# Kernel tuning notes

Measured on AMD Instinct MI355X. Metric: run time of the kernel, lower is better.

Reference implementation:

```python
import jax, jax.numpy as jnp
import numpy as np
from jax.scipy.special import logsumexp

TEMPERATURE = 0.1
EPS = 1e-8  # matches torch F.cosine_similarity eps


def setup_inputs() -> dict:
    key = jax.random.key(0)
    k1, k2 = jax.random.split(key)
    N, D, NUM_CLASSES = 8192, 256, 64
    embeddings = jax.random.normal(k1, (N, D), dtype=jnp.float32)
    target = jax.random.randint(k2, (N,), 0, NUM_CLASSES, dtype=jnp.int64)
    return {"embeddings": embeddings, "target": target}


def reference(embeddings, target):
    N = target.shape[0]
    # cosine similarity: normalize rows, then a single GEMM for all pairs
    norms = jnp.linalg.norm(embeddings, axis=-1, keepdims=True)
    e = embeddings / jnp.maximum(norms, EPS)
    sim = (e @ e.T) / TEMPERATURE  # [N, N]

    pos = target[:, None] == target[None, :]  # [N, N] bool, incl. diagonal
    diag = jnp.eye(N, dtype=bool)
    neg_inf = jnp.asarray(-jnp.inf, dtype=sim.dtype)

    # denominator: negatives only (positives masked to -inf)
    lse_neg = logsumexp(jnp.where(pos, neg_inf, sim), axis=1)
    # numerator: positives excluding self (diagonal masked to -inf)
    lse_pos = logsumexp(jnp.where(pos & ~diag, sim, neg_inf), axis=1)

    loss = lse_neg - lse_pos
    return loss.sum()
```

## Files before the change

### kernel.cpp

```cpp
#include <hip/hip_runtime.h>
#include <hip/hip_bf16.h>
#include <stdint.h>
#include <math.h>

#define NROWS 8192
#define DIM   256
#define RB    256
#define BI    128
#define JSUB  64
#define NBJS  8
#define JBLK  (JSUB*NBJS)
#define NG    (NROWS/JBLK)
#define NIT   (NROWS/BI)
#define CAP   256

typedef __attribute__((ext_vector_type(4)))  int   int4v;
typedef __attribute__((ext_vector_type(8)))  int   int8v;
typedef __attribute__((ext_vector_type(16))) float floatx16;

typedef const __attribute__((address_space(1))) uint32_t gas_u32;
typedef __attribute__((address_space(3))) uint32_t las_u32;

#define SCALE_1_16 0x7B7B7B7B
#define L2E10      14.4269504088896f

#if __has_builtin(__builtin_amdgcn_exp2f)
#define EXP2(x) __builtin_amdgcn_exp2f(x)
#else
#define EXP2(x) exp2f(x)
#endif

__device__ __forceinline__ void gload_lds16(const void* g, void* l) {
    __builtin_amdgcn_global_load_lds((gas_u32*)(uintptr_t)g,
                                     (las_u32*)(uintptr_t)l, 16, 0, 0);
}

__global__ __launch_bounds__(256) void normalize_kernel(const float* __restrict__ emb,
                                                        uint32_t* __restrict__ e8,
                                                        float* __restrict__ out)
{
    if (blockIdx.x == 0 && threadIdx.x == 0) *out = 0.f;
    int row  = blockIdx.x * 4 + (threadIdx.x >> 6);
    int lane = threadIdx.x & 63;
    const float4* rowp = (const float4*)(emb + (size_t)row * DIM);
    float4 v = rowp[lane];
    float ss = v.x*v.x + v.y*v.y + v.z*v.z + v.w*v.w;
    #pragma unroll
    for (int off = 32; off > 0; off >>= 1)
        ss += __shfl_xor(ss, off, 64);
    float inv = 16.0f / fmaxf(sqrtf(ss), 1e-8f);
    int r = __builtin_amdgcn_cvt_pk_fp8_f32(v.x * inv, v.y * inv, 0, false);
    r     = __builtin_amdgcn_cvt_pk_fp8_f32(v.z * inv, v.w * inv, r, true);
    e8[(size_t)row * (DIM / 4) + lane] = (uint32_t)r;
}

__global__ __launch_bounds__(256) void pos_kernel(const uint8_t* __restrict__ e8,
                                                  const int* __restrict__ tgt,
                                                  float* __restrict__ sp)
{
    __shared__ uint8_t rows[CAP * RB];
    __shared__ int idx[CAP];
    __shared__ int cnt;

    const int c    = blockIdx.x;
    const int tid  = threadIdx.x;
    const int wave = tid >> 6;
    const int lane = tid & 63;
    const int col  = lane & 31;
    const int h    = lane >> 5;

    if (tid == 0) cnt = 0;
    __syncthreads();
    for (int base = 0; base < NROWS; base += 256) {
        int j = base + tid;
        if (tgt[j] == c) {
            int p = atomicAdd(&cnt, 1);
            if (p < CAP) idx[p] = j;
        }
    }
    __syncthreads();
    const int M  = min(cnt, CAP);
    const int Mp = (M + 31) & ~31;

    const int nslots = M * 16;
    for (int g = wave; g * 64 < nslots; g += 4) {
        int s  = g * 64 + lane;
        int r  = s >> 4;
        int rc = min(r, M - 1);
        int lc = (s & 15) ^ (r & 15);
        gload_lds16(e8 + (size_t)idx[rc] * RB + lc * 16, rows + g * 1024);
    }
    __syncthreads();
    for (int s = M * 16 + tid; s < Mp * 16; s += 256)
        *(int4v*)(rows + (size_t)s * 16) = (int4v){0, 0, 0, 0};
    __syncthreads();

    const int xm = col & 15;
    int poff[4];
    #pragma unroll
    for (int s = 0; s < 4; ++s)
        poff[s] = ((s * 4 + h * 2) ^ xm) << 4;

    for (int bt = wave; bt * 32 < Mp; bt += 4) {
        const int b = bt * 32 + col;
        const uint8_t* pb = rows + (size_t)b * RB;
        int8v bfr[4];
        #pragma unroll
        for (int s = 0; s < 4; ++s) {
            int4v lo = *(const int4v*)(pb + poff[s]);
            int4v hi = *(const int4v*)(pb + (poff[s] ^ 16));
            bfr[s] = __builtin_shufflevector(lo, hi, 0, 1, 2, 3, 4, 5, 6, 7);
        }
        float psum = 0.f;
        for (int at = 0; at * 32 < Mp; ++at) {
            const uint8_t* pa = rows + (size_t)(at * 32 + col) * RB;
            floatx16 acc = (floatx16){0.f,0.f,0.f,0.f,0.f,0.f,0.f,0.f,
                                      0.f,0.f,0.f,0.f,0.f,0.f,0.f,0.f};
            #pragma unroll
            for (int s = 0; s < 4; ++s) {
                int4v lo = *(const int4v*)(pa + poff[s]);
                int4v hi = *(const int4v*)(pa + (poff[s] ^ 16));
                int8v af = __builtin_shufflevector(lo, hi, 0, 1, 2, 3, 4, 5, 6, 7);
                acc = __builtin_amdgcn_mfma_scale_f32_32x32x64_f8f6f4(
                    af, bfr[s], acc, 0, 0, 0, SCALE_1_16, 0, SCALE_1_16);
            }
            #pragma unroll
            for (int rq = 0; rq < 4; ++rq)
                #pragma unroll
                for (int r2 = 0; r2 < 4; ++r2) {
                    const int a = at * 32 + rq * 8 + h * 4 + r2;
                    float v = EXP2(fmaf(L2E10, acc[rq * 4 + r2], -L2E10));
                    psum += (a != b && a < M) ? v : 0.f;
                }
        }
        psum += __shfl_xor(psum, 32, 64);
        if (h == 0 && b < M) sp[idx[b]] = psum;
    }
}

template<bool DIAG>
__device__ __forceinline__ void epi(const floatx16 acc[2],
                                    int jbs, int h, int ic0, float& ts)
{
    #pragma unroll
    for (int jt = 0; jt < 2; ++jt)
        #pragma unroll
        for (int rq = 0; rq < 4; ++rq)
            #pragma unroll
            for (int r2 = 0; r2 < 4; ++r2) {
                float v = EXP2(fmaf(L2E10, acc[jt][rq * 4 + r2], -L2E10));
                if (DIAG) {
                    const int jg_ = jbs + jt * 32 + rq * 8 + h * 4 + r2;
                    if (jg_ == ic0) v = 0.f;
                }
                ts += v;
            }
}

__global__ __launch_bounds__(256, 4) void tile_kernel(const uint8_t* __restrict__ e8,
                                                      float* __restrict__ pts)
{
    __shared__ uint8_t buf[2][JSUB * RB];

    const int bi   = blockIdx.x;
    const int jg   = blockIdx.y;
    const int tid  = threadIdx.x;
    const int wave = tid >> 6;
    const int lane = tid & 63;
    const int col  = lane & 31;
    const int h    = lane >> 5;

    const uint8_t* pb = e8 + (size_t)(bi * BI + wave * 32 + col) * RB + h * 32;
    int8v bfr[4];
    #pragma unroll
    for (int s = 0; s < 4; ++s)
        bfr[s] = *(const int8v*)(pb + s * 64);

    int goffA[4];
    #pragma unroll
    for (int t = 0; t < 4; ++t) {
        int s   = wave * 256 + t * 64 + lane;
        int row = s >> 4;
        int lc  = (s & 15) ^ (row & 15);
        goffA[t] = row * RB + lc * 16;
    }
    const char* gA = (const char*)(e8 + (size_t)jg * JBLK * RB);

    #pragma unroll
    for (int t = 0; t < 4; ++t)
        gload_lds16(gA + goffA[t], buf[0] + wave * 4096 + t * 1024);

    const int ic0 = bi * BI + wave * 32 + col;

    const int xm = col & 15;
    int poff[4];
    #pragma unroll
    for (int s = 0; s < 4; ++s)
        poff[s] = ((s * 4 + h * 2) ^ xm) << 4;

    __syncthreads();

    float ts = 0.f;
    const int dpair = bi - jg * 4;

    #pragma unroll
    for (int bjs = 0; bjs < NBJS; ++bjs) {
        if (bjs < NBJS - 1) {
            const char* gAn = gA + (size_t)(bjs + 1) * JSUB * RB;
            #pragma unroll
            for (int t = 0; t < 4; ++t)
                gload_lds16(gAn + goffA[t], buf[(bjs + 1) & 1] + wave * 4096 + t * 1024);
        }

        const uint8_t* ab = buf[bjs & 1];
        floatx16 acc[2];
        #pragma unroll
        for (int jt = 0; jt < 2; ++jt)
            acc[jt] = (floatx16){0.f,0.f,0.f,0.f,0.f,0.f,0.f,0.f,
                                 0.f,0.f,0.f,0.f,0.f,0.f,0.f,0.f};

        #pragma unroll
        for (int s = 0; s < 4; ++s) {
            int8v af[2];
            #pragma unroll
            for (int jt = 0; jt < 2; ++jt) {
                const uint8_t* pa = ab + (size_t)(jt * 32 + col) * RB;
                int4v lo = *(const int4v*)(pa + poff[s]);
                int4v hi = *(const int4v*)(pa + (poff[s] ^ 16));
                af[jt] = __builtin_shufflevector(lo, hi, 0, 1, 2, 3, 4, 5, 6, 7);
            }
            #pragma unroll
            for (int jt = 0; jt < 2; ++jt)
                acc[jt] = __builtin_amdgcn_mfma_scale_f32_32x32x64_f8f6f4(
                    af[jt], bfr[s], acc[jt], 0, 0,
                    0, SCALE_1_16, 0, SCALE_1_16);
        }

        const int jbs = jg * JBLK + bjs * JSUB;
        if ((bjs >> 1) == dpair)
            epi<true >(acc, jbs, h, ic0, ts);
        else
            epi<false>(acc, jbs, h, ic0, ts);

        if (bjs < NBJS - 1)
            __syncthreads();
    }

    ts += __shfl_xor(ts, 32, 64);
    if (h == 0)
        pts[(size_t)jg * NROWS + ic0] = ts;
}

__global__ __launch_bounds__(256) void finalize_kernel(const float* __restrict__ pts,
                                                       const float* __restrict__ sp,
                                                       float* __restrict__ out)
{
    const int i = blockIdx.x * 256 + threadIdx.x;
    float st = 0.f;
    #pragma unroll
    for (int t = 0; t < NG; ++t)
        st += pts[(size_t)t * NROWS + i];
    const float spv = sp[i];
    const float ns  = st - spv;
    float loss = logf(ns) - logf(spv);
    #pragma unroll
    for (int off = 32; off > 0; off >>= 1)
        loss += __shfl_xor(loss, off, 64);
    __shared__ float w4[4];
    if ((threadIdx.x & 63) == 0) w4[threadIdx.x >> 6] = loss;
    __syncthreads();
    if (threadIdx.x == 0)
        atomicAdd(out, w4[0] + w4[1] + w4[2] + w4[3]);
}

extern "C" void kernel_launch(void* const* d_in, const int* in_sizes, int n_in,
                              void* d_out, int out_size, void* d_ws, size_t ws_size,
                              hipStream_t stream)
{
    (void)in_sizes; (void)n_in; (void)out_size; (void)ws_size;
    const float* emb = (const float*)d_in[0];
    const int*   tgt = (const int*)d_in[1];
    float*       out = (float*)d_out;

    uint32_t* e8  = (uint32_t*)d_ws;
    float*    pts = (float*)((char*)d_ws + (size_t)NROWS * RB);
    float*    sp  = pts + (size_t)NG * NROWS;

    normalize_kernel<<<NROWS / 4, 256, 0, stream>>>(emb, e8, out);

    pos_kernel<<<64, 256, 0, stream>>>((const uint8_t*)e8, tgt, sp);

    dim3 grid(NIT, NG);
    tile_kernel<<<grid, 256, 0, stream>>>((const uint8_t*)e8, pts);

    finalize_kernel<<<NROWS / 256, 256, 0, stream>>>(pts, sp, out);
}
```

Before: 98.61 us.

## Fuse positive-pair kernel into tile kernel and fold exp scaling into FP8 operands

Merges the per-class positive-sum kernel into the main similarity tile kernel as 64 extra blocks, removing one launch and letting positive work run alongside the negative tiles. Normalization now writes two FP8 copies, one pre-scaled by log2(e)/T so the epilogue becomes a bare exp2 with no FMA. The positive path now reads operands directly from global/L2 instead of staging them in LDS. The trade-offs are coarser quantization of the scaled A copy, roughly fp8 e4m3 precision on values up to about 230, and double the FP8 workspace writes. The exp offset of -1/T is also dropped, which is algebraically safe because the shift cancels in lse_neg minus lse_pos.

```diff
diff --git a/kernel.cpp b/kernel.cpp
--- a/kernel.cpp
+++ b/kernel.cpp
@@ -12,6 +12,7 @@
 #define JBLK  (JSUB*NBJS)
 #define NG    (NROWS/JBLK)
 #define NIT   (NROWS/BI)
+#define NCLS  64
 #define CAP   256
 
 typedef __attribute__((ext_vector_type(4)))  int   int4v;
@@ -23,6 +24,8 @@
 
 #define SCALE_1_16 0x7B7B7B7B
 #define L2E10      14.4269504088896f
+#define CA_SCALE   (L2E10 * 16.0f)
+#define CB_SCALE   16.0f
 
 #if __has_builtin(__builtin_amdgcn_exp2f)
 #define EXP2(x) __builtin_amdgcn_exp2f(x)
@@ -36,106 +39,26 @@
 }
 
 __global__ __launch_bounds__(256) void normalize_kernel(const float* __restrict__ emb,
-                                                        uint32_t* __restrict__ e8,
+                                                        uint32_t* __restrict__ a8,
+                                                        uint32_t* __restrict__ b8,
                                                         float* __restrict__ out)
 {
     if (blockIdx.x == 0 && threadIdx.x == 0) *out = 0.f;
     int row  = blockIdx.x * 4 + (threadIdx.x >> 6);
     int lane = threadIdx.x & 63;
-    const float4* rowp = (const float4*)(emb + (size_t)row * DIM);
-    float4 v = rowp[lane];
+    float4 v = ((const float4*)(emb + (size_t)row * DIM))[lane];
     float ss = v.x*v.x + v.y*v.y + v.z*v.z + v.w*v.w;
     #pragma unroll
     for (int off = 32; off > 0; off >>= 1)
         ss += __shfl_xor(ss, off, 64);
-    float inv = 16.0f / fmaxf(sqrtf(ss), 1e-8f);
-    int r = __builtin_amdgcn_cvt_pk_fp8_f32(v.x * inv, v.y * inv, 0, false);
-    r     = __builtin_amdgcn_cvt_pk_fp8_f32(v.z * inv, v.w * inv, r, true);
-    e8[(size_t)row * (DIM / 4) + lane] = (uint32_t)r;
-}
-
-__global__ __launch_bounds__(256) void pos_kernel(const uint8_t* __restrict__ e8,
-                                                  const int* __restrict__ tgt,
-                                                  float* __restrict__ sp)
-{
-    __shared__ uint8_t rows[CAP * RB];
-    __shared__ int idx[CAP];
-    __shared__ int cnt;
-
-    const int c    = blockIdx.x;
-    const int tid  = threadIdx.x;
-    const int wave = tid >> 6;
-    const int lane = tid & 63;
-    const int col  = lane & 31;
-    const int h    = lane >> 5;
-
-    if (tid == 0) cnt = 0;
-    __syncthreads();
-    for (int base = 0; base < NROWS; base += 256) {
-        int j = base + tid;
-        if (tgt[j] == c) {
-            int p = atomicAdd(&cnt, 1);
-            if (p < CAP) idx[p] = j;
-        }
-    }
-    __syncthreads();
-    const int M  = min(cnt, CAP);
-    const int Mp = (M + 31) & ~31;
-
-    const int nslots = M * 16;
-    for (int g = wave; g * 64 < nslots; g += 4) {
-        int s  = g * 64 + lane;
-        int r  = s >> 4;
-        int rc = min(r, M - 1);
-        int lc = (s & 15) ^ (r & 15);
-        gload_lds16(e8 + (size_t)idx[rc] * RB + lc * 16, rows + g * 1024);
-    }
-    __syncthreads();
-    for (int s = M * 16 + tid; s < Mp * 16; s += 256)
-        *(int4v*)(rows + (size_t)s * 16) = (int4v){0, 0, 0, 0};
-    __syncthreads();
-
-    const int xm = col & 15;
-    int poff[4];
-    #pragma unroll
-    for (int s = 0; s < 4; ++s)
-        poff[s] = ((s * 4 + h * 2) ^ xm) << 4;
-
-    for (int bt = wave; bt * 32 < Mp; bt += 4) {
-        const int b = bt * 32 + col;
-        const uint8_t* pb = rows + (size_t)b * RB;
-        int8v bfr[4];
-        #pragma unroll
-        for (int s = 0; s < 4; ++s) {
-            int4v lo = *(const int4v*)(pb + poff[s]);
-            int4v hi = *(const int4v*)(pb + (poff[s] ^ 16));
-            bfr[s] = __builtin_shufflevector(lo, hi, 0, 1, 2, 3, 4, 5, 6, 7);
-        }
-        float psum = 0.f;
-        for (int at = 0; at * 32 < Mp; ++at) {
-            const uint8_t* pa = rows + (size_t)(at * 32 + col) * RB;
-            floatx16 acc = (floatx16){0.f,0.f,0.f,0.f,0.f,0.f,0.f,0.f,
-                                      0.f,0.f,0.f,0.f,0.f,0.f,0.f,0.f};
-            #pragma unroll
-            for (int s = 0; s < 4; ++s) {
-                int4v lo = *(const int4v*)(pa + poff[s]);
-                int4v hi = *(const int4v*)(pa + (poff[s] ^ 16));
-                int8v af = __builtin_shufflevector(lo, hi, 0, 1, 2, 3, 4, 5, 6, 7);
-                acc = __builtin_amdgcn_mfma_scale_f32_32x32x64_f8f6f4(
-                    af, bfr[s], acc, 0, 0, 0, SCALE_1_16, 0, SCALE_1_16);
-            }
-            #pragma unroll
-            for (int rq = 0; rq < 4; ++rq)
-                #pragma unroll
-                for (int r2 = 0; r2 < 4; ++r2) {
-                    const int a = at * 32 + rq * 8 + h * 4 + r2;
-                    float v = EXP2(fmaf(L2E10, acc[rq * 4 + r2], -L2E10));
-                    psum += (a != b && a < M) ? v : 0.f;
-                }
-        }
-        psum += __shfl_xor(psum, 32, 64);
-        if (h == 0 && b < M) sp[idx[b]] = psum;
-    }
+    float inv = 1.0f / fmaxf(sqrtf(ss), 1e-8f);
+    float ia = CA_SCALE * inv, ib = CB_SCALE * inv;
+    int ra = __builtin_amdgcn_cvt_pk_fp8_f32(v.x * ia, v.y * ia, 0, false);
+    ra     = __builtin_amdgcn_cvt_pk_fp8_f32(v.z * ia, v.w * ia, ra, true);
+    int rb = __builtin_amdgcn_cvt_pk_fp8_f32(v.x * ib, v.y * ib, 0, false);
+    rb     = __builtin_amdgcn_cvt_pk_fp8_f32(v.z * ib, v.w * ib, rb, true);
+    a8[(size_t)row * 64 + lane] = (uint32_t)ra;
+    b8[(size_t)row * 64 + lane] = (uint32_t)rb;
 }
 
 template<bool DIAG>
@@ -148,7 +71,7 @@
         for (int rq = 0; rq < 4; ++rq)
             #pragma unroll
             for (int r2 = 0; r2 < 4; ++r2) {
-                float v = EXP2(fmaf(L2E10, acc[jt][rq * 4 + r2], -L2E10));
+                float v = EXP2(acc[jt][rq * 4 + r2]);
                 if (DIAG) {
                     const int jg_ = jbs + jt * 32 + rq * 8 + h * 4 + r2;
                     if (jg_ == ic0) v = 0.f;
@@ -157,20 +80,81 @@
             }
 }
 
-__global__ __launch_bounds__(256, 4) void tile_kernel(const uint8_t* __restrict__ e8,
-                                                      float* __restrict__ pts)
-{
-    __shared__ uint8_t buf[2][JSUB * RB];
-
-    const int bi   = blockIdx.x;
-    const int jg   = blockIdx.y;
+__global__ __launch_bounds__(256, 4) void fused_kernel(const uint8_t* __restrict__ eA,
+                                                       const uint8_t* __restrict__ eB,
+                                                       const int* __restrict__ tgt,
+                                                       float* __restrict__ pts,
+                                                       float* __restrict__ sp)
+{
+    __shared__ uint8_t smem[2 * JSUB * RB];
+
     const int tid  = threadIdx.x;
     const int wave = tid >> 6;
     const int lane = tid & 63;
     const int col  = lane & 31;
     const int h    = lane >> 5;
 
-    const uint8_t* pb = e8 + (size_t)(bi * BI + wave * 32 + col) * RB + h * 32;
+    if (blockIdx.x < NCLS) {
+        int* idx = (int*)smem;
+        int* cnt = (int*)(smem + CAP * 4);
+        const int c = blockIdx.x;
+        if (tid == 0) *cnt = 0;
+        __syncthreads();
+        int4v tv[8];
+        #pragma unroll
+        for (int k = 0; k < 8; ++k)
+            tv[k] = *(const int4v*)(tgt + k * 1024 + tid * 4);
+        #pragma unroll
+        for (int k = 0; k < 8; ++k)
+            #pragma unroll
+            for (int r = 0; r < 4; ++r)
+                if (tv[k][r] == c) {
+                    int p = atomicAdd(cnt, 1);
+                    if (p < CAP) idx[p] = k * 1024 + tid * 4 + r;
+                }
+        __syncthreads();
+        const int M   = min(*cnt, CAP);
+        const int Mp  = (M + 31) & ~31;
+        const int nbt = Mp >> 5;
+
+        for (int bt = wave; bt < nbt; bt += 4) {
+            const int b = bt * 32 + col;
+            const uint8_t* pb = eB + (size_t)idx[min(b, M - 1)] * RB + h * 32;
+            int8v bfr[4];
+            #pragma unroll
+            for (int s = 0; s < 4; ++s)
+                bfr[s] = *(const int8v*)(pb + s * 64);
+            float psum = 0.f;
+            for (int at = 0; at < nbt; ++at) {
+                const uint8_t* pa = eA + (size_t)idx[min(at * 32 + col, M - 1)] * RB + h * 32;
+                floatx16 acc = (floatx16){0.f,0.f,0.f,0.f,0.f,0.f,0.f,0.f,
+                                          0.f,0.f,0.f,0.f,0.f,0.f,0.f,0.f};
+                #pragma unroll
+                for (int s = 0; s < 4; ++s) {
+                    int8v af = *(const int8v*)(pa + s * 64);
+                    acc = __builtin_amdgcn_mfma_scale_f32_32x32x64_f8f6f4(
+                        af, bfr[s], acc, 0, 0, 0, SCALE_1_16, 0, SCALE_1_16);
+                }
+                #pragma unroll
+                for (int rq = 0; rq < 4; ++rq)
+                    #pragma unroll
+                    for (int r2 = 0; r2 < 4; ++r2) {
+                        const int a = at * 32 + rq * 8 + h * 4 + r2;
+                        float v = EXP2(acc[rq * 4 + r2]);
+                        psum += (a != b && a < M) ? v : 0.f;
+                    }
+            }
+            psum += __shfl_xor(psum, 32, 64);
+            if (h == 0 && b < M) sp[idx[b]] = psum;
+        }
+        return;
+    }
+
+    const int g  = blockIdx.x - NCLS;
+    const int bi = g & (NIT - 1);
+    const int jg = g >> 6;
+
+    const uint8_t* pb = eB + (size_t)(bi * BI + wave * 32 + col) * RB + h * 32;
     int8v bfr[4];
     #pragma unroll
     for (int s = 0; s < 4; ++s)
@@ -184,11 +168,11 @@
         int lc  = (s & 15) ^ (row & 15);
         goffA[t] = row * RB + lc * 16;
     }
-    const char* gA = (const char*)(e8 + (size_t)jg * JBLK * RB);
+    const char* gA = (const char*)(eA + (size_t)jg * JBLK * RB);
 
     #pragma unroll
     for (int t = 0; t < 4; ++t)
-        gload_lds16(gA + goffA[t], buf[0] + wave * 4096 + t * 1024);
+        gload_lds16(gA + goffA[t], smem + wave * 4096 + t * 1024);
 
     const int ic0 = bi * BI + wave * 32 + col;
 
@@ -209,10 +193,11 @@
             const char* gAn = gA + (size_t)(bjs + 1) * JSUB * RB;
             #pragma unroll
             for (int t = 0; t < 4; ++t)
-                gload_lds16(gAn + goffA[t], buf[(bjs + 1) & 1] + wave * 4096 + t * 1024);
+                gload_lds16(gAn + goffA[t],
+                            smem + ((bjs + 1) & 1) * (JSUB * RB) + wave * 4096 + t * 1024);
         }
 
-        const uint8_t* ab = buf[bjs & 1];
+        const uint8_t* ab = smem + (bjs & 1) * (JSUB * RB);
         floatx16 acc[2];
         #pragma unroll
         for (int jt = 0; jt < 2; ++jt)
@@ -282,16 +267,15 @@
     const int*   tgt = (const int*)d_in[1];
     float*       out = (float*)d_out;
 
-    uint32_t* e8  = (uint32_t*)d_ws;
-    float*    pts = (float*)((char*)d_ws + (size_t)NROWS * RB);
+    uint32_t* a8  = (uint32_t*)d_ws;
+    uint32_t* b8  = a8 + (size_t)NROWS * 64;
+    float*    pts = (float*)(b8 + (size_t)NROWS * 64);
     float*    sp  = pts + (size_t)NG * NROWS;
 
-    normalize_kernel<<<NROWS / 4, 256, 0, stream>>>(emb, e8, out);
-
-    pos_kernel<<<64, 256, 0, stream>>>((const uint8_t*)e8, tgt, sp);
-
-    dim3 grid(NIT, NG);
-    tile_kernel<<<grid, 256, 0, stream>>>((const uint8_t*)e8, pts);
+    normalize_kernel<<<NROWS / 4, 256, 0, stream>>>(emb, a8, b8, out);
+
+    fused_kernel<<<NCLS + NIT * NG, 256, 0, stream>>>(
+        (const uint8_t*)a8, (const uint8_t*)b8, tgt, pts, sp);
 
     finalize_kernel<<<NROWS / 256, 256, 0, stream>>>(pts, sp, out);
 }
```

New measurement: 83.01 us. -15.8%, faster.
